# Optimization experiments

Hardware: AMD Instinct MI355X
Metric: run time of the kernel (lower is better)

## Reference

```python
import jax, jax.numpy as jnp
import numpy as np

EPS = 1e-8  # torch F.cosine_similarity default eps


def setup_inputs() -> dict:
    key = jax.random.key(0)
    k1, k2 = jax.random.split(key)
    x = jax.random.normal(k1, (16384, 1024), dtype=jnp.float32)
    label = jax.random.randint(k2, (16384, 64), 0, 2).astype(jnp.int64)
    w = jnp.asarray(10.0, dtype=jnp.float32)  # nn.Parameter init_w
    b = jnp.asarray(-5.0, dtype=jnp.float32)  # nn.Parameter init_b
    return {"x": x, "label": label, "w": w, "b": b}


def reference(x, label, w, b):
    # Append the 'no-label' column for rows whose label vector is all zero.
    extra = (label.sum(axis=1) == 0).astype(label.dtype)[:, None]
    lab = jnp.concatenate([label, extra], axis=1).astype(x.dtype)  # [B, C]

    counts = lab.sum(axis=0)                  # [C] positives per centroid
    active = counts > 0                       # torch drops empty columns; we mask them

    # Centroids: mean of x over rows carrying each label (scatter-mean as GEMM).
    anchor = (lab.T @ x) / jnp.maximum(counts, 1.0)[:, None]   # [C, D]

    # Cosine similarity between every sample and every centroid.
    xn = jnp.maximum(jnp.linalg.norm(x, axis=1), EPS)          # [B]
    an = jnp.maximum(jnp.linalg.norm(anchor, axis=1), EPS)     # [C]
    cos = (x @ anchor.T) / (xn[:, None] * an[None, :])          # [B, C]

    logits = cos * w + b
    # Removing empty columns from softmax == setting their logits to -inf.
    logits = jnp.where(active[None, :], logits, -jnp.inf)
    logp = jax.nn.log_softmax(logits, axis=1)                   # [B, C]

    # Row expansion in torch duplicates sample i once per positive label j;
    # the logits row only depends on i, so CE over expanded rows is a
    # pair-weighted mean of -logp[i, j] over positive (i, j) pairs.
    n_pairs = lab.sum()
    nloss = -jnp.sum(jnp.where(lab > 0, logp, 0.0)) / n_pairs
    return nloss
```

## Files before the change

### kernel.cpp

```cpp
#include <hip/hip_runtime.h>
#include <hip/hip_bf16.h>
#include <stdint.h>

#define NROWS 16384
#define NDIM  1024
#define NLAB  64
#define NC    65
#define CPAD  80

typedef float float4v __attribute__((ext_vector_type(4)));
typedef short short8  __attribute__((ext_vector_type(8)));

static constexpr size_t SCALE_B = 0;
static constexpr size_t ACTB_B  = 320;
static constexpr size_t CNTF_B  = 448;
static constexpr size_t CNTP_B  = 1024;
static constexpr size_t MASK_B  = 83968;
static constexpr size_t XN2_B   = 215040;
static constexpr size_t LFRAG_B = 280576;
static constexpr size_t BFRAG_B = 2902016;
static constexpr size_t XAF_B   = 3065856;
static constexpr size_t PART_B  = 36620288;
static constexpr size_t SLAB    = (size_t)CPAD * NDIM * 4;
static constexpr size_t WARR_B  = 60000256;

__device__ __forceinline__ unsigned short bf16u(float f) {
    __hip_bfloat16 h = __float2bfloat16(f);
    return __builtin_bit_cast(unsigned short, h);
}
__device__ __forceinline__ unsigned pk2(float a, float b) {
    return (unsigned)bf16u(a) | ((unsigned)bf16u(b) << 16);
}

__global__ __launch_bounds__(256) void kA_labels(const int* __restrict__ label,
                                                 unsigned long long* __restrict__ masks,
                                                 unsigned* __restrict__ cntpart,
                                                 unsigned short* __restrict__ lfrag) {
    __shared__ unsigned cnt[NC];
    __shared__ unsigned long long smask[64];
    int t = threadIdx.x;
    int bid = blockIdx.x;
    if (t < NC) cnt[t] = 0;
    __syncthreads();
    int wave = t >> 6, lane = t & 63;
    int rowblock = bid * 64;
    unsigned creg = 0, zreg = 0;
#pragma unroll 4
    for (int p = 0; p < 16; ++p) {
        int row = rowblock + p * 4 + wave;
        int v = label[row * NLAB + lane];
        unsigned long long m = __ballot(v != 0);
        creg += (unsigned)((m >> lane) & 1ull);
        if (lane == 0) {
            masks[row] = m;
            smask[p * 4 + wave] = m;
            zreg += (m == 0ull) ? 1u : 0u;
        }
    }
    atomicAdd(&cnt[lane], creg);
    if (lane == 0 && zreg) atomicAdd(&cnt[64], zreg);
    __syncthreads();
    if (t < 80) cntpart[bid * 80 + t] = (t < NC) ? cnt[t] : 0u;
    for (int pid = t; pid < 640; pid += 256) {
        int rt2l = pid / 320, rem = pid % 320;
        int ct = rem >> 6, ln = rem & 63;
        int qq = ln >> 4, cc = ln & 15;
        int c = ct * 16 + cc;
        int rbase = rt2l * 32 + qq * 8;
        unsigned pk[4];
#pragma unroll
        for (int jp = 0; jp < 4; ++jp) {
            unsigned long long m0 = smask[rbase + jp * 2], m1 = smask[rbase + jp * 2 + 1];
            unsigned b0, b1;
            if (c < 64)       { b0 = (unsigned)((m0 >> c) & 1ull); b1 = (unsigned)((m1 >> c) & 1ull); }
            else if (c == 64) { b0 = (m0 == 0ull); b1 = (m1 == 0ull); }
            else              { b0 = 0u; b1 = 0u; }
            pk[jp] = (b0 ? 0x3F80u : 0u) | (b1 ? 0x3F800000u : 0u);
        }
        uint4 w = make_uint4(pk[0], pk[1], pk[2], pk[3]);
        ((uint4*)lfrag)[((size_t)(bid * 2 + rt2l) * 5 + ct) * 64 + ln] = w;
    }
}

__global__ __launch_bounds__(256) void kBP(const float* __restrict__ x,
                                           const unsigned short* __restrict__ lfrag,
                                           float* __restrict__ partial,
                                           unsigned short* __restrict__ xAfrag,
                                           float* __restrict__ xn2g,
                                           int kslices) {
    __shared__ float xt[2][32][65];
    __shared__ float red2[4][16];
    int t = threadIdx.x, wave = t >> 6, lane = t & 63;
    int q = lane >> 4, col = lane & 15;
    int ngemm = 16 * kslices;

    if ((int)blockIdx.x >= ngemm) {
        int rt = blockIdx.x - ngemm;
        const float* rowp = x + ((size_t)rt * 16 + col) * NDIM;
        uint4* dst = (uint4*)xAfrag + ((size_t)rt * 32 + wave * 8) * 64 + lane;
        float4 fa[8], fb[8];
#pragma unroll
        for (int kb = 0; kb < 8; ++kb) {
            int d0 = wave * 256 + kb * 32 + q * 8;
            fa[kb] = *(const float4*)(rowp + d0);
            fb[kb] = *(const float4*)(rowp + d0 + 4);
        }
        float sq = 0.f;
#pragma unroll
        for (int kb = 0; kb < 8; ++kb) {
            sq += fa[kb].x * fa[kb].x + fa[kb].y * fa[kb].y + fa[kb].z * fa[kb].z + fa[kb].w * fa[kb].w
                + fb[kb].x * fb[kb].x + fb[kb].y * fb[kb].y + fb[kb].z * fb[kb].z + fb[kb].w * fb[kb].w;
            uint4 v;
            v.x = pk2(fa[kb].x, fa[kb].y); v.y = pk2(fa[kb].z, fa[kb].w);
            v.z = pk2(fb[kb].x, fb[kb].y); v.w = pk2(fb[kb].z, fb[kb].w);
            dst[kb * 64] = v;
        }
        sq += __shfl_xor(sq, 16, 64);
        sq += __shfl_xor(sq, 32, 64);
        if (q == 0) red2[wave][col] = sq;
        __syncthreads();
        if (t < 16) xn2g[rt * 16 + t] = red2[0][t] + red2[1][t] + red2[2][t] + red2[3][t];
        return;
    }

    int dgroup = blockIdx.x & 15, ks = blockIdx.x >> 4;
    int nkb = (NROWS / kslices) >> 5;
    int kb0 = ks * nkb;
    int d = dgroup * 64 + wave * 16 + col;
    const uint4* A = (const uint4*)lfrag;
    int srow = t >> 3, sd = (t & 7) * 8;

    float4v acc[5];
#pragma unroll
    for (int ct = 0; ct < 5; ++ct) acc[ct] = (float4v){0.f, 0.f, 0.f, 0.f};

    {
        const float* g = x + ((size_t)(kb0 * 32 + srow)) * NDIM + dgroup * 64 + sd;
        float4 u = *(const float4*)g, v2 = *(const float4*)(g + 4);
        float* L = &xt[0][srow][sd];
        L[0] = u.x; L[1] = u.y; L[2] = u.z; L[3] = u.w;
        L[4] = v2.x; L[5] = v2.y; L[6] = v2.z; L[7] = v2.w;
    }
    __syncthreads();

    for (int i = 0; i < nkb; ++i) {
        int cur = i & 1;
        float4 u, v2;
        bool havenext = (i + 1) < nkb;
        if (havenext) {
            const float* g = x + ((size_t)((kb0 + i + 1) * 32 + srow)) * NDIM + dgroup * 64 + sd;
            u = *(const float4*)g; v2 = *(const float4*)(g + 4);
        }
        int kb = kb0 + i;
        uint4 a0[5];
#pragma unroll
        for (int ct = 0; ct < 5; ++ct) a0[ct] = A[((size_t)kb * 5 + ct) * 64 + lane];
        float f[8];
#pragma unroll
        for (int j = 0; j < 8; ++j) f[j] = xt[cur][q * 8 + j][wave * 16 + col];
        uint4 bq;
        bq.x = pk2(f[0], f[1]); bq.y = pk2(f[2], f[3]);
        bq.z = pk2(f[4], f[5]); bq.w = pk2(f[6], f[7]);
        short8 bf = __builtin_bit_cast(short8, bq);
#pragma unroll
        for (int ct = 0; ct < 5; ++ct) {
            short8 af = __builtin_bit_cast(short8, a0[ct]);
            acc[ct] = __builtin_amdgcn_mfma_f32_16x16x32_bf16(af, bf, acc[ct], 0, 0, 0);
        }
        if (havenext) {
            float* L = &xt[cur ^ 1][srow][sd];
            L[0] = u.x; L[1] = u.y; L[2] = u.z; L[3] = u.w;
            L[4] = v2.x; L[5] = v2.y; L[6] = v2.z; L[7] = v2.w;
        }
        __syncthreads();
    }
    float* pb = partial + (size_t)ks * CPAD * NDIM;
#pragma unroll
    for (int ct = 0; ct < 5; ++ct)
#pragma unroll
        for (int reg = 0; reg < 4; ++reg)
            pb[(size_t)(ct * 16 + q * 4 + reg) * NDIM + d] = acc[ct][reg];
}

__global__ __launch_bounds__(1024) void kC_fuse(const float* __restrict__ wptr,
                                                const unsigned* __restrict__ cntpart,
                                                const float* __restrict__ partial,
                                                int kslices,
                                                unsigned short* __restrict__ bfrag,
                                                float* __restrict__ scale,
                                                unsigned char* __restrict__ actB,
                                                unsigned* __restrict__ countsF) {
    int c = blockIdx.x, t = threadIdx.x;
    __shared__ float red[16];
    __shared__ unsigned credu[4];
    __shared__ float bcast[1];
    if (t < 256) {
        unsigned cv = cntpart[t * 80 + c];
#pragma unroll
        for (int m = 32; m >= 1; m >>= 1) cv += __shfl_xor(cv, m, 64);
        if ((t & 63) == 0) credu[t >> 6] = cv;
    }
    const float* p = partial + (size_t)c * NDIM + t;
    float s = 0.f;
#pragma unroll 8
    for (int sl = 0; sl < kslices; ++sl) s += p[(size_t)sl * CPAD * NDIM];
    float ss = s * s;
#pragma unroll
    for (int m = 32; m >= 1; m >>= 1) ss += __shfl_xor(ss, m, 64);
    if ((t & 63) == 0) red[t >> 6] = ss;
    __syncthreads();
    if (t == 0) {
        float tot = 0.f;
#pragma unroll
        for (int j = 0; j < 16; ++j) tot += red[j];
        bcast[0] = sqrtf(tot);
    }
    unsigned cnt = credu[0] + credu[1] + credu[2] + credu[3];
    __syncthreads();
    float invc = 1.0f / (float)(cnt > 0u ? cnt : 1u);
    float a = s * invc;
    float an = fmaxf(bcast[0] * invc, 1e-8f);
    unsigned short h = bf16u(a / an);
    int ct = c >> 4, colc = c & 15;
    int kb = t >> 5, q = (t >> 3) & 3, j0 = t & 7;
    bfrag[((((size_t)ct * 32 + kb) * 64) + q * 16 + colc) * 8 + j0] = h;
    float hv = __bfloat162float(__builtin_bit_cast(__hip_bfloat16, h));
    float nb2 = hv * hv;
#pragma unroll
    for (int m = 32; m >= 1; m >>= 1) nb2 += __shfl_xor(nb2, m, 64);
    if ((t & 63) == 0) red[t >> 6] = nb2;
    __syncthreads();
    if (t == 0) {
        float n2 = 0.f;
#pragma unroll
        for (int j = 0; j < 16; ++j) n2 += red[j];
        scale[c] = (n2 > 0.f) ? (wptr[0] / sqrtf(n2)) : 0.f;
        actB[c] = (cnt > 0u) ? 1 : 0;
        countsF[c] = cnt;
    }
}

__global__ __launch_bounds__(256) void k3_loss(const unsigned short* __restrict__ xAfrag,
                                               const unsigned short* __restrict__ bfrag,
                                               const float* __restrict__ xn2g,
                                               const unsigned long long* __restrict__ masks,
                                               const unsigned char* __restrict__ actB,
                                               const float* __restrict__ scale,
                                               const float* __restrict__ bptr,
                                               float* __restrict__ wsumArr) {
    __shared__ float redsm[3][64][21];
    int t = threadIdx.x, wave = t >> 6, lane = t & 63;
    int q = lane >> 4, col = lane & 15;
    int rt = blockIdx.x;
    int rowbase = rt * 16;
    const uint4* A = (const uint4*)xAfrag + (size_t)rt * 32 * 64 + lane;
    const uint4* Bp = (const uint4*)bfrag + lane;
    int kb0 = wave * 8;

    float4v acc[5];
#pragma unroll
    for (int ct = 0; ct < 5; ++ct) acc[ct] = (float4v){0.f, 0.f, 0.f, 0.f};

    uint4 a[8];
#pragma unroll
    for (int j = 0; j < 8; ++j) a[j] = A[(size_t)(kb0 + j) * 64];
    uint4 b0[5], b1[5];
#pragma unroll
    for (int ct = 0; ct < 5; ++ct) b0[ct] = Bp[(size_t)(ct * 32 + kb0 + 0) * 64];
#pragma unroll
    for (int ct = 0; ct < 5; ++ct) b1[ct] = Bp[(size_t)(ct * 32 + kb0 + 1) * 64];

    for (int s = 0; s < 8; s += 2) {
        int p2 = s + 2 < 8 ? kb0 + s + 2 : kb0 + s;
        int p3 = s + 3 < 8 ? kb0 + s + 3 : kb0 + s + 1;
        {
            short8 af = __builtin_bit_cast(short8, a[s]);
#pragma unroll
            for (int ct = 0; ct < 5; ++ct) {
                short8 bf = __builtin_bit_cast(short8, b0[ct]);
                acc[ct] = __builtin_amdgcn_mfma_f32_16x16x32_bf16(af, bf, acc[ct], 0, 0, 0);
            }
#pragma unroll
            for (int ct = 0; ct < 5; ++ct) b0[ct] = Bp[(size_t)(ct * 32 + p2) * 64];
        }
        {
            short8 af = __builtin_bit_cast(short8, a[s + 1]);
#pragma unroll
            for (int ct = 0; ct < 5; ++ct) {
                short8 bf = __builtin_bit_cast(short8, b1[ct]);
                acc[ct] = __builtin_amdgcn_mfma_f32_16x16x32_bf16(af, bf, acc[ct], 0, 0, 0);
            }
#pragma unroll
            for (int ct = 0; ct < 5; ++ct) b1[ct] = Bp[(size_t)(ct * 32 + p3) * 64];
        }
    }

    if (wave) {
#pragma unroll
        for (int ct = 0; ct < 5; ++ct)
#pragma unroll
            for (int reg = 0; reg < 4; ++reg)
                redsm[wave - 1][lane][ct * 4 + reg] = acc[ct][reg];
    }
    __syncthreads();
    if (wave != 0) return;
#pragma unroll
    for (int w = 0; w < 3; ++w)
#pragma unroll
        for (int ct = 0; ct < 5; ++ct)
#pragma unroll
            for (int reg = 0; reg < 4; ++reg)
                acc[ct][reg] += redsm[w][lane][ct * 4 + reg];

    float bv = bptr[0];
    float sc[5]; unsigned char ab[5];
#pragma unroll
    for (int ct = 0; ct < 5; ++ct) { sc[ct] = scale[ct * 16 + col]; ab[ct] = actB[ct * 16 + col]; }

    float contrib = 0.f;
#pragma unroll
    for (int reg = 0; reg < 4; ++reg) {
        int rl = q * 4 + reg;
        int row = rowbase + rl;
        float inv = 1.0f / fmaxf(sqrtf(xn2g[row]), 1e-8f);
        unsigned long long mask = masks[row];
        float v[5]; float lmax = -1e30f;
#pragma unroll
        for (int ct = 0; ct < 5; ++ct) {
            float lg = acc[ct][reg] * sc[ct] * inv + bv;
            v[ct] = ab[ct] ? lg : -1e30f;
            lmax = fmaxf(lmax, v[ct]);
        }
#pragma unroll
        for (int m = 1; m < 16; m <<= 1) lmax = fmaxf(lmax, __shfl_xor(lmax, m, 16));
        float es = 0.f;
#pragma unroll
        for (int ct = 0; ct < 5; ++ct) es += __expf(v[ct] - lmax);
#pragma unroll
        for (int m = 1; m < 16; m <<= 1) es += __shfl_xor(es, m, 16);
        float lse = lmax + __logf(es);
        float ps = 0.f;
#pragma unroll
        for (int ct = 0; ct < 5; ++ct) {
            int c = ct * 16 + col;
            bool pos = (c < 64) ? (((mask >> c) & 1ull) != 0ull)
                                : ((c == 64) ? (mask == 0ull) : false);
            ps += pos ? v[ct] : 0.f;
        }
#pragma unroll
        for (int m = 1; m < 16; m <<= 1) ps += __shfl_xor(ps, m, 16);
        float npos = mask ? (float)__popcll(mask) : 1.0f;
        float crow = ps - npos * lse;
        if (col == 0) contrib += crow;
    }
#pragma unroll
    for (int m = 1; m < 64; m <<= 1) contrib += __shfl_xor(contrib, m, 64);
    if (lane == 0) wsumArr[rt] = contrib;
}

__global__ __launch_bounds__(256) void kE_final(const float* __restrict__ wsumArr,
                                                const unsigned* __restrict__ countsF,
                                                float* __restrict__ out) {
    __shared__ float red[4];
    int t = threadIdx.x, wave = t >> 6, lane = t & 63;
    float s = wsumArr[t] + wsumArr[t + 256] + wsumArr[t + 512] + wsumArr[t + 768];
#pragma unroll
    for (int m = 32; m >= 1; m >>= 1) s += __shfl_xor(s, m, 64);
    if (lane == 0) red[wave] = s;
    __syncthreads();
    if (t == 0) {
        float wv = red[0] + red[1] + red[2] + red[3];
        float np = 0.f;
        for (int c = 0; c < NC; ++c) np += (float)countsF[c];
        out[0] = -wv / np;
    }
}

extern "C" void kernel_launch(void* const* d_in, const int* in_sizes, int n_in,
                              void* d_out, int out_size, void* d_ws, size_t ws_size,
                              hipStream_t stream) {
    (void)in_sizes; (void)n_in; (void)out_size;
    const float* x = (const float*)d_in[0];
    const int* label = (const int*)d_in[1];
    const float* w = (const float*)d_in[2];
    const float* b = (const float*)d_in[3];

    char* ws = (char*)d_ws;
    float* scale = (float*)(ws + SCALE_B);
    unsigned char* actB = (unsigned char*)(ws + ACTB_B);
    unsigned* countsF = (unsigned*)(ws + CNTF_B);
    unsigned* cntpart = (unsigned*)(ws + CNTP_B);
    unsigned long long* masks = (unsigned long long*)(ws + MASK_B);
    float* xn2g = (float*)(ws + XN2_B);
    unsigned short* lfrag = (unsigned short*)(ws + LFRAG_B);
    unsigned short* bfrag = (unsigned short*)(ws + BFRAG_B);
    unsigned short* xAfrag = (unsigned short*)(ws + XAF_B);
    float* partial = (float*)(ws + PART_B);
    float* wsumArr = (float*)(ws + WARR_B);

    int kslices = 64;
    while (kslices > 8 && PART_B + (size_t)kslices * SLAB > WARR_B) kslices >>= 1;
    (void)ws_size;

    hipLaunchKernelGGL(kA_labels, dim3(256), dim3(256), 0, stream,
                       label, masks, cntpart, lfrag);
    hipLaunchKernelGGL(kBP, dim3(16 * kslices + 1024), dim3(256), 0, stream,
                       x, lfrag, partial, xAfrag, xn2g, kslices);
    hipLaunchKernelGGL(kC_fuse, dim3(CPAD), dim3(1024), 0, stream,
                       w, cntpart, partial, kslices, bfrag, scale, actB, countsF);
    hipLaunchKernelGGL(k3_loss, dim3(NROWS / 16), dim3(256), 0, stream,
                       xAfrag, bfrag, xn2g, masks, actB, scale, b, wsumArr);
    hipLaunchKernelGGL(kE_final, dim3(1), dim3(256), 0, stream,
                       wsumArr, countsF, (float*)d_out);
}
```

Baseline: 147.7 us.

## Fuse bf16 repack and row-norm computation into centroid GEMM tile loop

The separate 1024 row-repack blocks are dropped, so x is no longer read twice. The GEMM blocks already stage x tiles in shared memory, and they now also write the bf16 A-fragments and per-dgroup partial squared norms from those tiles. The 16 per-row partial norms are summed later in kC_fuse. This saves a full pass over x (64MB) but adds LDS reads, global stores and ALU work inside the GEMM's inner loop, plus an extra partial-norm buffer.

Result: no change. 146.9 us (-0.6%).

```diff
diff --git a/kernel.cpp b/kernel.cpp
--- a/kernel.cpp
+++ b/kernel.cpp
@@ -23,6 +23,7 @@
 static constexpr size_t PART_B  = 36620288;
 static constexpr size_t SLAB    = (size_t)CPAD * NDIM * 4;
 static constexpr size_t WARR_B  = 60000256;
+static constexpr size_t XN2P_B  = 61000192;
 
 __device__ __forceinline__ unsigned short bf16u(float f) {
     __hip_bfloat16 h = __float2bfloat16(f);
@@ -82,47 +83,16 @@
     }
 }
 
-__global__ __launch_bounds__(256) void kBP(const float* __restrict__ x,
-                                           const unsigned short* __restrict__ lfrag,
-                                           float* __restrict__ partial,
-                                           unsigned short* __restrict__ xAfrag,
-                                           float* __restrict__ xn2g,
-                                           int kslices) {
+__global__ __launch_bounds__(256) void kG(const float* __restrict__ x,
+                                          const unsigned short* __restrict__ lfrag,
+                                          float* __restrict__ partial,
+                                          unsigned short* __restrict__ xAfrag,
+                                          float* __restrict__ xn2p,
+                                          int kslices) {
     __shared__ float xt[2][32][65];
-    __shared__ float red2[4][16];
+    __shared__ float sqacc[2][32][8];
     int t = threadIdx.x, wave = t >> 6, lane = t & 63;
     int q = lane >> 4, col = lane & 15;
-    int ngemm = 16 * kslices;
-
-    if ((int)blockIdx.x >= ngemm) {
-        int rt = blockIdx.x - ngemm;
-        const float* rowp = x + ((size_t)rt * 16 + col) * NDIM;
-        uint4* dst = (uint4*)xAfrag + ((size_t)rt * 32 + wave * 8) * 64 + lane;
-        float4 fa[8], fb[8];
-#pragma unroll
-        for (int kb = 0; kb < 8; ++kb) {
-            int d0 = wave * 256 + kb * 32 + q * 8;
-            fa[kb] = *(const float4*)(rowp + d0);
-            fb[kb] = *(const float4*)(rowp + d0 + 4);
-        }
-        float sq = 0.f;
-#pragma unroll
-        for (int kb = 0; kb < 8; ++kb) {
-            sq += fa[kb].x * fa[kb].x + fa[kb].y * fa[kb].y + fa[kb].z * fa[kb].z + fa[kb].w * fa[kb].w
-                + fb[kb].x * fb[kb].x + fb[kb].y * fb[kb].y + fb[kb].z * fb[kb].z + fb[kb].w * fb[kb].w;
-            uint4 v;
-            v.x = pk2(fa[kb].x, fa[kb].y); v.y = pk2(fa[kb].z, fa[kb].w);
-            v.z = pk2(fb[kb].x, fb[kb].y); v.w = pk2(fb[kb].z, fb[kb].w);
-            dst[kb * 64] = v;
-        }
-        sq += __shfl_xor(sq, 16, 64);
-        sq += __shfl_xor(sq, 32, 64);
-        if (q == 0) red2[wave][col] = sq;
-        __syncthreads();
-        if (t < 16) xn2g[rt * 16 + t] = red2[0][t] + red2[1][t] + red2[2][t] + red2[3][t];
-        return;
-    }
-
     int dgroup = blockIdx.x & 15, ks = blockIdx.x >> 4;
     int nkb = (NROWS / kslices) >> 5;
     int kb0 = ks * nkb;
@@ -130,6 +100,13 @@
     const uint4* A = (const uint4*)lfrag;
     int srow = t >> 3, sd = (t & 7) * 8;
 
+    int rh = t >> 7;
+    int kbh = (t >> 6) & 1;
+    int qq = (t >> 4) & 3;
+    int cc = t & 15;
+    int r2 = rh * 16 + cc;
+    int dch = kbh * 4 + qq;
+
     float4v acc[5];
 #pragma unroll
     for (int ct = 0; ct < 5; ++ct) acc[ct] = (float4v){0.f, 0.f, 0.f, 0.f};
@@ -145,6 +122,12 @@
 
     for (int i = 0; i < nkb; ++i) {
         int cur = i & 1;
+        if (i > 0 && t < 32) {
+            float s8 = 0.f;
+#pragma unroll
+            for (int d2 = 0; d2 < 8; ++d2) s8 += sqacc[(i - 1) & 1][t][d2];
+            xn2p[(size_t)dgroup * NROWS + (size_t)(kb0 + i - 1) * 32 + t] = s8;
+        }
         float4 u, v2;
         bool havenext = (i + 1) < nkb;
         if (havenext) {
@@ -167,12 +150,32 @@
             short8 af = __builtin_bit_cast(short8, a0[ct]);
             acc[ct] = __builtin_amdgcn_mfma_f32_16x16x32_bf16(af, bf, acc[ct], 0, 0, 0);
         }
+        {
+            float g0[8];
+#pragma unroll
+            for (int j = 0; j < 8; ++j) g0[j] = xt[cur][r2][dch * 8 + j];
+            float sp = 0.f;
+#pragma unroll
+            for (int j = 0; j < 8; ++j) sp += g0[j] * g0[j];
+            sqacc[cur][r2][dch] = sp;
+            uint4 v;
+            v.x = pk2(g0[0], g0[1]); v.y = pk2(g0[2], g0[3]);
+            v.z = pk2(g0[4], g0[5]); v.w = pk2(g0[6], g0[7]);
+            size_t slot = (((size_t)kb * 2 + rh) * 32 + dgroup * 2 + kbh) * 64 + (t & 63);
+            ((uint4*)xAfrag)[slot] = v;
+        }
         if (havenext) {
             float* L = &xt[cur ^ 1][srow][sd];
             L[0] = u.x; L[1] = u.y; L[2] = u.z; L[3] = u.w;
             L[4] = v2.x; L[5] = v2.y; L[6] = v2.z; L[7] = v2.w;
         }
         __syncthreads();
+    }
+    if (t < 32) {
+        float s8 = 0.f;
+#pragma unroll
+        for (int d2 = 0; d2 < 8; ++d2) s8 += sqacc[(nkb - 1) & 1][t][d2];
+        xn2p[(size_t)dgroup * NROWS + (size_t)(kb0 + nkb - 1) * 32 + t] = s8;
     }
     float* pb = partial + (size_t)ks * CPAD * NDIM;
 #pragma unroll
@@ -189,7 +192,9 @@
                                                 unsigned short* __restrict__ bfrag,
                                                 float* __restrict__ scale,
                                                 unsigned char* __restrict__ actB,
-                                                unsigned* __restrict__ countsF) {
+                                                unsigned* __restrict__ countsF,
+                                                const float* __restrict__ xn2p,
+                                                float* __restrict__ xn2g) {
     int c = blockIdx.x, t = threadIdx.x;
     __shared__ float red[16];
     __shared__ unsigned credu[4];
@@ -199,6 +204,13 @@
 #pragma unroll
         for (int m = 32; m >= 1; m >>= 1) cv += __shfl_xor(cv, m, 64);
         if ((t & 63) == 0) credu[t >> 6] = cv;
+    }
+    int gid = c * 1024 + t;
+    if (gid < NROWS) {
+        float s2 = 0.f;
+#pragma unroll
+        for (int dg = 0; dg < 16; ++dg) s2 += xn2p[(size_t)dg * NROWS + gid];
+        xn2g[gid] = s2;
     }
     const float* p = partial + (size_t)c * NDIM + t;
     float s = 0.f;
@@ -397,6 +409,7 @@
     unsigned short* xAfrag = (unsigned short*)(ws + XAF_B);
     float* partial = (float*)(ws + PART_B);
     float* wsumArr = (float*)(ws + WARR_B);
+    float* xn2p = (float*)(ws + XN2P_B);
 
     int kslices = 64;
     while (kslices > 8 && PART_B + (size_t)kslices * SLAB > WARR_B) kslices >>= 1;
@@ -404,10 +417,10 @@
 
     hipLaunchKernelGGL(kA_labels, dim3(256), dim3(256), 0, stream,
                        label, masks, cntpart, lfrag);
-    hipLaunchKernelGGL(kBP, dim3(16 * kslices + 1024), dim3(256), 0, stream,
-                       x, lfrag, partial, xAfrag, xn2g, kslices);
+    hipLaunchKernelGGL(kG, dim3(16 * kslices), dim3(256), 0, stream,
+                       x, lfrag, partial, xAfrag, xn2p, kslices);
     hipLaunchKernelGGL(kC_fuse, dim3(CPAD), dim3(1024), 0, stream,
-                       w, cntpart, partial, kslices, bfrag, scale, actB, countsF);
+                       w, cntpart, partial, kslices, bfrag, scale, actB, countsF, xn2p, xn2g);
     hipLaunchKernelGGL(k3_loss, dim3(NROWS / 16), dim3(256), 0, stream,
                        xAfrag, bfrag, xn2g, masks, actB, scale, b, wsumArr);
     hipLaunchKernelGGL(kE_final, dim3(1), dim3(256), 0, stream,
```
